# Kernel optimization log

Hardware: AMD Instinct MI355X
Metric: run time of the kernel (lower is better)

## Reference

```python
import jax, jax.numpy as jnp
import numpy as np

B, G, D, N_HEADS, FFN, L = 16, 2048, 256, 8, 1024, 4
HEAD_DIM = D // N_HEADS
EPS_LN = 1e-5
MASK_TOKEN = -10.0
REE_BASE = 100.0


def setup_inputs() -> dict:
    key = jax.random.key(0)
    ks = jax.random.split(key, 20)
    s = 0.02
    inp = {
        'x': jax.random.normal(ks[0], (B, G), jnp.float32),
        'gene_emb': jax.random.normal(ks[1], (G, D), jnp.float32) * s,
        'inv_freq': (1.0 / REE_BASE ** (jnp.arange(0, D, 2, dtype=jnp.float32) / D)),
        'Wq': jax.random.normal(ks[2], (L, D, D), jnp.float32) * s,
        'bq': jnp.zeros((L, D), jnp.float32),
        'Wk': jax.random.normal(ks[3], (L, D, D), jnp.float32) * s,
        'bk': jnp.zeros((L, D), jnp.float32),
        'Wv': jax.random.normal(ks[4], (L, D, D), jnp.float32) * s,
        'bv': jnp.zeros((L, D), jnp.float32),
        'ln1_g': jnp.ones((L, D), jnp.float32),
        'ln1_b': jnp.zeros((L, D), jnp.float32),
        'ln2_g': jnp.ones((L, D), jnp.float32),
        'ln2_b': jnp.zeros((L, D), jnp.float32),
        'WU': jax.random.normal(ks[5], (L, D, FFN), jnp.float32) * s,
        'bU': jnp.zeros((L, FFN), jnp.float32),
        'WV': jax.random.normal(ks[6], (L, FFN, D), jnp.float32) * s,
        'bV': jnp.zeros((L, D), jnp.float32),
        'Wout': jax.random.normal(ks[7], (D, 1), jnp.float32) * s,
        'bout': jnp.zeros((1,), jnp.float32),
    }
    return inp


def layernorm(x, g, b):
    m = x.mean(-1, keepdims=True)
    v = ((x - m) ** 2).mean(-1, keepdims=True)
    return (x - m) / jnp.sqrt(v + EPS_LN) * g + b


def causal_linear_attention(q, k, v):
    # q, k already feature-mapped ('sqr'); shapes [B, S, H, dh]
    b, s, h, dh = q.shape
    qs, ks_, vs = (jnp.moveaxis(t, 1, 0) for t in (q, k, v))  # [S,B,H,dh]
    num0 = jnp.zeros((b, h, dh, dh), q.dtype)
    den0 = jnp.zeros((b, h, dh), q.dtype)

    def step(carry, qkv):
        num_s, den_s = carry
        qt, kt, vt = qkv
        num_s = num_s + jnp.einsum('bhf,bhd->bhfd', kt, vt)
        den_s = den_s + kt
        num = jnp.einsum('bhf,bhfd->bhd', qt, num_s)
        den = jnp.einsum('bhf,bhf->bh', qt, den_s)
        return (num_s, den_s), num / (den[..., None] + 1e-16)

    _, out = jax.lax.scan(step, (num0, den0), (qs, ks_, vs))  # [S,B,H,dh]
    return jnp.moveaxis(out, 0, 1).reshape(b, s, h * dh)


def reference(x, gene_emb, inv_freq, Wq, bq, Wk, bk, Wv, bv,
              ln1_g, ln1_b, ln2_g, ln2_b, WU, bU, WV, bV, Wout, bout):
    b, g = x.shape
    # Rotary Expression Embedding
    freqs = x[..., None] * inv_freq  # [B,G,D/2]
    emb = jnp.concatenate([jnp.sin(freqs), jnp.cos(freqs)], axis=-1)  # [B,G,D]
    emb = jnp.where((x == MASK_TOKEN)[..., None], 0.0, emb)
    h = gene_emb[None] + emb  # [B,G,D]

    for l in range(Wq.shape[0]):
        hn = layernorm(h, ln1_g[l], ln1_b[l])  # pre-LN (on_gptln=True)
        q = (hn @ Wq[l] + bq[l]).reshape(b, g, N_HEADS, HEAD_DIM) ** 2
        k = (hn @ Wk[l] + bk[l]).reshape(b, g, N_HEADS, HEAD_DIM) ** 2
        v = (hn @ Wv[l] + bv[l]).reshape(b, g, N_HEADS, HEAD_DIM)
        h = h + causal_linear_attention(q, k, v)
        hn2 = layernorm(h, ln2_g[l], ln2_b[l])
        h = h + jax.nn.gelu(hn2 @ WU[l] + bU[l], approximate=False) @ WV[l] + bV[l]
    return (h @ Wout + bout).squeeze(-1)  # [B,G]
```

## Files before the change

kernel.cpp:

```cpp
#include <hip/hip_runtime.h>
#include <math.h>


#define GG 2048
#define DD 256
#define NROWS 32768
#define NC 32
#define CS 64

typedef __attribute__((ext_vector_type(8))) short bf16x8;
typedef __attribute__((ext_vector_type(4))) float f32x4;

struct FalseT { static constexpr bool value = false; };
struct TrueT  { static constexpr bool value = true;  };

__device__ __forceinline__ short f2bf(float f) {
  union { float f; unsigned u; } v; v.f = f;
  unsigned r = v.u + 0x7FFFu + ((v.u >> 16) & 1u);
  return (short)(r >> 16);
}
__device__ __forceinline__ float bf2f(short s) {
  union { unsigned u; float f; } v; v.u = ((unsigned)(unsigned short)s) << 16;
  return v.f;
}
__device__ __forceinline__ void gld16(const short* g, short* l) {
  __builtin_amdgcn_global_load_lds(
      (const __attribute__((address_space(1))) void*)g,
      (__attribute__((address_space(3))) void*)l, 16, 0, 0);
}
__device__ __forceinline__ float fast_gelu(float x) {
  float y = 1.595769122f * (x + 0.044715f * x * x * x);
  return x / (1.0f + __expf(-y));
}

__global__ __launch_bounds__(256) void embed_kernel(
    const float* __restrict__ x, const float* __restrict__ ge,
    const float* __restrict__ invf, float* __restrict__ h) {
  int bg = blockIdx.x * 4 + (threadIdx.x >> 6);
  int g = bg & (GG - 1);
  int lane = threadIdx.x & 63;
  float xv = x[bg];
  int d = lane * 4;
  float4 e;
  if (lane < 32) {
    float4 f = *(const float4*)&invf[d];
    e.x = sinf(xv * f.x); e.y = sinf(xv * f.y);
    e.z = sinf(xv * f.z); e.w = sinf(xv * f.w);
  } else {
    float4 f = *(const float4*)&invf[d - 128];
    e.x = cosf(xv * f.x); e.y = cosf(xv * f.y);
    e.z = cosf(xv * f.z); e.w = cosf(xv * f.w);
  }
  if (xv == -10.0f) { e.x = 0.f; e.y = 0.f; e.z = 0.f; e.w = 0.f; }
  float4 gv = *(const float4*)&ge[(size_t)g * DD + d];
  float4 o; o.x = gv.x + e.x; o.y = gv.y + e.y; o.z = gv.z + e.z; o.w = gv.w + e.w;
  *(float4*)&h[(size_t)bg * DD + d] = o;
}

__global__ __launch_bounds__(256) void ln_tiled(
    const float* __restrict__ h, const float* __restrict__ gamma,
    const float* __restrict__ beta, short* __restrict__ outT) {
  __shared__ float mean_s[32], rstd_s[32];
  __shared__ float gls[256], bls[256];
  int r0 = blockIdx.x * 32;
  int tid = threadIdx.x;
  gls[tid] = gamma[tid]; bls[tid] = beta[tid];
  {
    int row = tid >> 3, seg = tid & 7;
    const float4* hp = (const float4*)(h + (size_t)(r0 + row) * DD + seg * 32);
    float s = 0.f, s2 = 0.f;
#pragma unroll
    for (int i = 0; i < 8; ++i) {
      float4 v = hp[i];
      s += v.x + v.y + v.z + v.w;
      s2 += v.x * v.x + v.y * v.y + v.z * v.z + v.w * v.w;
    }
    s += __shfl_xor(s, 1); s += __shfl_xor(s, 2); s += __shfl_xor(s, 4);
    s2 += __shfl_xor(s2, 1); s2 += __shfl_xor(s2, 2); s2 += __shfl_xor(s2, 4);
    if (seg == 0) {
      float mn = s * (1.0f / 256.0f);
      mean_s[row] = mn;
      rstd_s[row] = rsqrtf(s2 * (1.0f / 256.0f) - mn * mn + 1e-5f);
    }
  }
  __syncthreads();
  int row = tid & 31, kc8 = (tid >> 5) & 3, half = tid >> 7;
  float mn = mean_s[row], rs = rstd_s[row];
  size_t hrow = (size_t)(r0 + row) * DD;
  int trow = (r0 & 127) + row;
  short* tb = outT + (size_t)(r0 >> 7) * 8 * 4096 + (kc8 * 128 + trow) * 8;
#pragma unroll
  for (int j = 0; j < 4; ++j) {
    int kb = half * 4 + j;
    int k0 = kb * 32 + kc8 * 8;
    float4 x0 = *(const float4*)&h[hrow + k0];
    float4 x1 = *(const float4*)&h[hrow + k0 + 4];
    float4 g0 = *(const float4*)&gls[k0], g1 = *(const float4*)&gls[k0 + 4];
    float4 b0 = *(const float4*)&bls[k0], b1 = *(const float4*)&bls[k0 + 4];
    bf16x8 aw;
    aw[0] = f2bf((x0.x - mn) * rs * g0.x + b0.x);
    aw[1] = f2bf((x0.y - mn) * rs * g0.y + b0.y);
    aw[2] = f2bf((x0.z - mn) * rs * g0.z + b0.z);
    aw[3] = f2bf((x0.w - mn) * rs * g0.w + b0.w);
    aw[4] = f2bf((x1.x - mn) * rs * g1.x + b1.x);
    aw[5] = f2bf((x1.y - mn) * rs * g1.y + b1.y);
    aw[6] = f2bf((x1.z - mn) * rs * g1.z + b1.z);
    aw[7] = f2bf((x1.w - mn) * rs * g1.w + b1.w);
    *(bf16x8*)&tb[(size_t)kb * 4096] = aw;
  }
}

__global__ __launch_bounds__(256) void prep_weights(
    const float* __restrict__ Wq, const float* __restrict__ Wk,
    const float* __restrict__ Wv, const float* __restrict__ WU,
    const float* __restrict__ WV,
    short* __restrict__ TQ, short* __restrict__ TK, short* __restrict__ TV,
    short* __restrict__ TU, short* __restrict__ TVd) {
  int zz = blockIdx.z, l = blockIdx.y;
  const float* src; short* dst; int Kd, Nd;
  if (zz == 0) { src = Wq; dst = TQ; Kd = 256; Nd = 256; }
  else if (zz == 1) { src = Wk; dst = TK; Kd = 256; Nd = 256; }
  else if (zz == 2) { src = Wv; dst = TV; Kd = 256; Nd = 256; }
  else if (zz == 3) { src = WU; dst = TU; Kd = 256; Nd = 1024; }
  else { src = WV; dst = TVd; Kd = 1024; Nd = 256; }
  int tot = Kd * Nd;
  int e = blockIdx.x * 256 + threadIdx.x;
  if (e >= tot) return;
  int t = e >> 12;
  int cslot = (e >> 3) & 511;
  int elem = e & 7;
  int kc8 = cslot >> 7, rn = cslot & 127;
  int nKb = Kd >> 5;
  int nt = t / nKb, kb = t - nt * nKb;
  int n = nt * 128 + rn, k = kb * 32 + kc8 * 8 + elem;
  dst[(size_t)l * tot + e] = f2bf(src[(size_t)l * tot + (size_t)k * Nd + n]);
}

template <int K, int EPI>
__global__ __launch_bounds__(256) void gemm_t(
    const short* __restrict__ A, const short* __restrict__ B0,
    const short* __restrict__ B1, const short* __restrict__ B2,
    const float* __restrict__ bias0, const float* __restrict__ bias1,
    const float* __restrict__ bias2,
    short* __restrict__ o0, short* __restrict__ o1, short* __restrict__ o2,
    float* __restrict__ outf, int N) {
  __shared__ __align__(16) short L[24576];
  constexpr int nIter = K / 32;
  int z = blockIdx.z;
  const short* Bt = (z == 0) ? B0 : (z == 1) ? B1 : B2;
  const float* bias = (z == 0) ? bias0 : (z == 1) ? bias1 : bias2;
  short* outz = (z == 0) ? o0 : (z == 1) ? o1 : o2;
  int m0 = blockIdx.x * 128, n0 = blockIdx.y * 128;
  int tid = threadIdx.x;
  int lane = tid & 63, w = tid >> 6;
  int q = lane >> 4, r = lane & 15;
  int wm = (w >> 1) * 64, wn = (w & 1) * 64;
  const short* At = A + (size_t)blockIdx.x * nIter * 4096;
  const short* Btl = Bt + (size_t)blockIdx.y * nIter * 4096;
  f32x4 vzero = {0.f, 0.f, 0.f, 0.f};
  f32x4 acc[4][4];
#pragma unroll
  for (int i = 0; i < 4; ++i)
#pragma unroll
    for (int j = 0; j < 4; ++j) acc[i][j] = vzero;

  int c0 = tid * 8, c1 = (tid + 256) * 8;
#pragma unroll
  for (int g = 0; g < 3; ++g) {
    gld16(At + g * 4096 + c0, &L[g * 4096 + c0]);
    gld16(At + g * 4096 + c1, &L[g * 4096 + c1]);
    gld16(Btl + g * 4096 + c0, &L[12288 + g * 4096 + c0]);
    gld16(Btl + g * 4096 + c1, &L[12288 + g * 4096 + c1]);
  }

  int abase = (q * 128 + wm + r) * 8;
  int bbase = (q * 128 + wn + r) * 8;

#pragma unroll
  for (int gi = 0; gi < nIter; ++gi) {
    const int rem = nIter - 1 - gi;
    if (rem >= 2)      __builtin_amdgcn_s_waitcnt(0x0f78);
    else if (rem == 1) __builtin_amdgcn_s_waitcnt(0x0f74);
    else               __builtin_amdgcn_s_waitcnt(0x0f70);
    __builtin_amdgcn_s_barrier();
    __builtin_amdgcn_s_setprio(1);
    const int cur = gi % 3;
    const short* Asc = &L[cur * 4096];
    const short* Bsc = &L[12288 + cur * 4096];
    bf16x8 af[4], bfr[4];
#pragma unroll
    for (int mt = 0; mt < 4; ++mt)
      af[mt] = *(const bf16x8*)&Asc[abase + mt * 16 * 8];
#pragma unroll
    for (int nt = 0; nt < 4; ++nt)
      bfr[nt] = *(const bf16x8*)&Bsc[bbase + nt * 16 * 8];
#pragma unroll
    for (int mt = 0; mt < 4; ++mt)
#pragma unroll
      for (int nt = 0; nt < 4; ++nt)
        acc[mt][nt] = __builtin_amdgcn_mfma_f32_16x16x32_bf16(bfr[nt], af[mt], acc[mt][nt], 0, 0, 0);
    __builtin_amdgcn_s_setprio(0);
    __builtin_amdgcn_s_waitcnt(0xc07f);
    __builtin_amdgcn_s_barrier();
    if (gi + 3 < nIter) {
      size_t kn = (size_t)(gi + 3) * 4096;
      gld16(At + kn + c0, &L[cur * 4096 + c0]);
      gld16(At + kn + c1, &L[cur * 4096 + c1]);
      gld16(Btl + kn + c0, &L[12288 + cur * 4096 + c0]);
      gld16(Btl + kn + c1, &L[12288 + cur * 4096 + c1]);
    }
  }

  float4 bias4[4];
#pragma unroll
  for (int nt = 0; nt < 4; ++nt) bias4[nt] = *(const float4*)&bias[n0 + wn + nt * 16 + q * 4];

  if (EPI == 0) {
    short* T = L;
#pragma unroll
    for (int mt = 0; mt < 4; ++mt) {
      int ml = wm + mt * 16 + r;
#pragma unroll
      for (int nt = 0; nt < 4; ++nt) {
        f32x4 v = acc[mt][nt];
        v[0] += bias4[nt].x; v[1] += bias4[nt].y; v[2] += bias4[nt].z; v[3] += bias4[nt].w;
        if (z < 2) { v[0] *= v[0]; v[1] *= v[1]; v[2] *= v[2]; v[3] *= v[3]; }
        short4 pk; pk.x = f2bf(v[0]); pk.y = f2bf(v[1]); pk.z = f2bf(v[2]); pk.w = f2bf(v[3]);
        *(short4*)&T[ml * 132 + wn + nt * 16 + q * 4] = pk;
      }
    }
    __syncthreads();
#pragma unroll
    for (int t2 = 0; t2 < 2; ++t2) {
      int task = tid + t2 * 256;
      int row = task & 127, hl = task >> 7;
      size_t obase = ((size_t)((n0 >> 5) + hl) * NROWS + m0 + row) * 32;
#pragma unroll
      for (int j = 0; j < 4; ++j)
        *(bf16x8*)&outz[obase + j * 8] = *(const bf16x8*)&T[row * 132 + hl * 32 + j * 8];
    }
  } else if (EPI == 1) {
#pragma unroll
    for (int mt = 0; mt < 4; ++mt) {
      int ml = wm + mt * 16 + r;
#pragma unroll
      for (int nt = 0; nt < 4; ++nt) {
        f32x4 v = acc[mt][nt];
        v[0] += bias4[nt].x; v[1] += bias4[nt].y; v[2] += bias4[nt].z; v[3] += bias4[nt].w;
#pragma unroll
        for (int e = 0; e < 4; ++e) v[e] = fast_gelu(v[e]);
        short4 o; o.x = f2bf(v[0]); o.y = f2bf(v[1]); o.z = f2bf(v[2]); o.w = f2bf(v[3]);
        int n = n0 + wn + nt * 16 + q * 4;
        size_t ti = ((size_t)blockIdx.x * (N >> 5) + (n >> 5)) * 4096 +
                    (size_t)(((n >> 3) & 3) << 10) + (ml << 3) + (n & 7);
        *(short4*)&outz[ti] = o;
      }
    }
  } else {
    float* TF = (float*)L;
#pragma unroll
    for (int half = 0; half < 2; ++half) {
      __syncthreads();
      if ((w & 1) == half) {
#pragma unroll
        for (int mt = 0; mt < 4; ++mt) {
          int ml = wm + mt * 16 + r;
#pragma unroll
          for (int nt = 0; nt < 4; ++nt) {
            f32x4 v = acc[mt][nt];
            v[0] += bias4[nt].x; v[1] += bias4[nt].y; v[2] += bias4[nt].z; v[3] += bias4[nt].w;
            *(f32x4*)&TF[ml * 68 + nt * 16 + q * 4] = v;
          }
        }
      }
      __syncthreads();
      int row = tid >> 1, col = (tid & 1) * 32;
      size_t hoff = (size_t)(m0 + row) * N + n0 + half * 64 + col;
#pragma unroll
      for (int j = 0; j < 8; ++j) {
        float4 add = *(const float4*)&TF[row * 68 + col + j * 4];
        float4 cur4 = *(float4*)&outf[hoff + j * 4];
        cur4.x += add.x; cur4.y += add.y; cur4.z += add.z; cur4.w += add.w;
        *(float4*)&outf[hoff + j * 4] = cur4;
      }
    }
  }
}

__global__ __launch_bounds__(512) void ffn_fused(
    const short* __restrict__ A, const short* __restrict__ TUw,
    const short* __restrict__ TVw, const float* __restrict__ bUp,
    const float* __restrict__ bVp, float* __restrict__ h) {
  __shared__ __align__(16) short L[81920];
  int tid = threadIdx.x;
  int lane = tid & 63, w = tid >> 6;
  int q = lane >> 4, r = lane & 15;
  int wmU = (w >> 2) * 64, wnU = (w & 3) * 32;
  int wmD = (w >> 2) * 64, wnD = (w & 3) * 64;
  const short* At = A + (size_t)blockIdx.x * 32768;

#pragma unroll
  for (int i = 0; i < 8; ++i)
    gld16(At + (i * 512 + tid) * 8, &L[(i * 512 + tid) * 8]);

  auto issueFor = [&](int t) {
    short* dst = &L[49152 + (t & 1) * 16384];
    int ss = t >> 2, pp = t & 3;
    if (pp < 2) {
      const short* g0 = TUw + ((size_t)ss * 8 + pp * 4) * 4096;
#pragma unroll
      for (int i = 0; i < 4; ++i)
        gld16(g0 + (i * 512 + tid) * 8, dst + (i * 512 + tid) * 8);
    } else {
      int kbg0 = ss * 4 + (pp - 2) * 2;
#pragma unroll
      for (int kl = 0; kl < 2; ++kl) {
        gld16(TVw + (size_t)(kbg0 + kl) * 4096 + tid * 8,
              dst + kl * 8192 + tid * 8);
        gld16(TVw + (size_t)(32 + kbg0 + kl) * 4096 + tid * 8,
              dst + kl * 8192 + 4096 + tid * 8);
      }
    }
  };

  issueFor(0); issueFor(1);

  f32x4 vzero = {0.f, 0.f, 0.f, 0.f};
  f32x4 accm[4][2], acco[4][4];
#pragma unroll
  for (int mt = 0; mt < 4; ++mt) {
#pragma unroll
    for (int nt = 0; nt < 2; ++nt) accm[mt][nt] = vzero;
#pragma unroll
    for (int nt = 0; nt < 4; ++nt) acco[mt][nt] = vzero;
  }
  float4 b4[2];

  auto slice = [&](int s, auto lastc) {
    constexpr bool LAST = decltype(lastc)::value;
#pragma unroll
    for (int p = 0; p < 2; ++p) {
      int sig = s * 4 + p;
      __builtin_amdgcn_s_waitcnt(0x0f74);
      __builtin_amdgcn_s_barrier();
      __builtin_amdgcn_s_setprio(1);
      const short* Ws = &L[49152 + (sig & 1) * 16384];
#pragma unroll
      for (int kl = 0; kl < 4; ++kl) {
        int kb = p * 4 + kl;
        bf16x8 af[4], bfr[2];
#pragma unroll
        for (int mt = 0; mt < 4; ++mt)
          af[mt] = *(const bf16x8*)&L[kb * 4096 + (q * 128 + wmU + mt * 16 + r) * 8];
#pragma unroll
        for (int nt = 0; nt < 2; ++nt)
          bfr[nt] = *(const bf16x8*)&Ws[kl * 4096 + (q * 128 + wnU + nt * 16 + r) * 8];
#pragma unroll
        for (int mt = 0; mt < 4; ++mt)
#pragma unroll
          for (int nt = 0; nt < 2; ++nt)
            accm[mt][nt] = __builtin_amdgcn_mfma_f32_16x16x32_bf16(
                bfr[nt], af[mt], accm[mt][nt], 0, 0, 0);
      }
      __builtin_amdgcn_s_setprio(0);
      if (p == 1) {
#pragma unroll
        for (int mt = 0; mt < 4; ++mt) {
          int row = wmU + mt * 16 + r;
#pragma unroll
          for (int nt = 0; nt < 2; ++nt) {
            f32x4 v = accm[mt][nt];
            float4 bb = b4[nt];
            v[0] += bb.x; v[1] += bb.y; v[2] += bb.z; v[3] += bb.w;
            short4 pk;
            pk.x = f2bf(fast_gelu(v[0])); pk.y = f2bf(fast_gelu(v[1]));
            pk.z = f2bf(fast_gelu(v[2])); pk.w = f2bf(fast_gelu(v[3]));
            int kc8 = 2 * nt + (q >> 1);
            *(short4*)&L[32768 + (w & 3) * 4096 + (kc8 * 128 + row) * 8 + (q & 1) * 4] = pk;
            accm[mt][nt] = vzero;
          }
        }
      }
      __builtin_amdgcn_s_waitcnt(0xc07f);
      __builtin_amdgcn_s_barrier();
      if (p == 0) {
        b4[0] = *(const float4*)&bUp[s * 128 + wnU + q * 4];
        b4[1] = *(const float4*)&bUp[s * 128 + wnU + 16 + q * 4];
      }
      if (sig + 2 < 32) issueFor(sig + 2);
    }
#pragma unroll
    for (int p2 = 0; p2 < 2; ++p2) {
      int sig = s * 4 + 2 + p2;
      if (LAST && p2 == 1) __builtin_amdgcn_s_waitcnt(0x0f70);
      else                 __builtin_amdgcn_s_waitcnt(0x0f74);
      __builtin_amdgcn_s_barrier();
      __builtin_amdgcn_s_setprio(1);
      const short* Ws = &L[49152 + (sig & 1) * 16384];
#pragma unroll
      for (int kl = 0; kl < 2; ++kl) {
        int mtile = p2 * 2 + kl;
        bf16x8 am[4], bvf[4];
#pragma unroll
        for (int mt = 0; mt < 4; ++mt)
          am[mt] = *(const bf16x8*)&L[32768 + mtile * 4096 + (q * 128 + wmD + mt * 16 + r) * 8];
#pragma unroll
        for (int nt = 0; nt < 4; ++nt)
          bvf[nt] = *(const bf16x8*)&Ws[kl * 8192 + (wnD >> 7) * 4096 +
                                        (q * 128 + (wnD & 127) + nt * 16 + r) * 8];
#pragma unroll
        for (int mt = 0; mt < 4; ++mt)
#pragma unroll
          for (int nt = 0; nt < 4; ++nt)
            acco[mt][nt] = __builtin_amdgcn_mfma_f32_16x16x32_bf16(
                bvf[nt], am[mt], acco[mt][nt], 0, 0, 0);
      }
      __builtin_amdgcn_s_setprio(0);
      __builtin_amdgcn_s_waitcnt(0xc07f);
      __builtin_amdgcn_s_barrier();
      if (sig + 2 < 32) issueFor(sig + 2);
    }
  };

  for (int s = 0; s < 7; ++s) slice(s, FalseT{});
  slice(7, TrueT{});

  float4 bv4[4];
#pragma unroll
  for (int nt = 0; nt < 4; ++nt) bv4[nt] = *(const float4*)&bVp[wnD + nt * 16 + q * 4];
  float* TF = (float*)L;
#pragma unroll
  for (int mt = 0; mt < 4; ++mt) {
    int row = wmD + mt * 16 + r;
#pragma unroll
    for (int nt = 0; nt < 4; ++nt) {
      f32x4 v = acco[mt][nt];
      v[0] += bv4[nt].x; v[1] += bv4[nt].y; v[2] += bv4[nt].z; v[3] += bv4[nt].w;
      *(f32x4*)&TF[row * 260 + wnD + nt * 16 + q * 4] = v;
    }
  }
  __syncthreads();
  size_t hbase = ((size_t)blockIdx.x * 128 + w * 16) * DD;
#pragma unroll
  for (int j = 0; j < 16; ++j) {
    float4 add = *(const float4*)&TF[(w * 16 + j) * 260 + lane * 4];
    float4 c4 = *(float4*)&h[hbase + (size_t)j * DD + lane * 4];
    c4.x += add.x; c4.y += add.y; c4.z += add.z; c4.w += add.w;
    *(float4*)&h[hbase + (size_t)j * DD + lane * 4] = c4;
  }
}

__global__ __launch_bounds__(256) void attn_chunk_kv(
    const short* __restrict__ Kb, const short* __restrict__ Vb,
    float* __restrict__ St, float* __restrict__ Zc) {
  __shared__ short Kt[4][32 * 72];
  __shared__ short Vt[4][32 * 72];
  int wid = threadIdx.x >> 6;
  int blk = blockIdx.x * 4 + wid;
  int c = blk & (NC - 1), bh = blk >> 5;
  int b = bh >> 3, hh = bh & 7;
  int lane = threadIdx.x & 63, q = lane >> 4, r = lane & 15;
  size_t rowbase = ((size_t)hh * NROWS + b * GG + c * CS + lane) * 32;
#pragma unroll
  for (int j = 0; j < 4; ++j) {
    bf16x8 kv = *(const bf16x8*)&Kb[rowbase + j * 8];
    bf16x8 vv = *(const bf16x8*)&Vb[rowbase + j * 8];
#pragma unroll
    for (int e = 0; e < 8; ++e) {
      Kt[wid][(j * 8 + e) * 72 + lane] = kv[e];
      Vt[wid][(j * 8 + e) * 72 + lane] = vv[e];
    }
  }
  __syncthreads();
  f32x4 vzero = {0.f, 0.f, 0.f, 0.f};
  f32x4 acc[2][2];
#pragma unroll
  for (int i = 0; i < 2; ++i)
#pragma unroll
    for (int j = 0; j < 2; ++j) acc[i][j] = vzero;
#pragma unroll
  for (int ks = 0; ks < 2; ++ks) {
    bf16x8 afr[2], bfr[2];
#pragma unroll
    for (int mt = 0; mt < 2; ++mt) afr[mt] = *(const bf16x8*)&Kt[wid][(mt * 16 + r) * 72 + ks * 32 + q * 8];
#pragma unroll
    for (int nt = 0; nt < 2; ++nt) bfr[nt] = *(const bf16x8*)&Vt[wid][(nt * 16 + r) * 72 + ks * 32 + q * 8];
#pragma unroll
    for (int mt = 0; mt < 2; ++mt)
#pragma unroll
      for (int nt = 0; nt < 2; ++nt)
        acc[mt][nt] = __builtin_amdgcn_mfma_f32_16x16x32_bf16(afr[mt], bfr[nt], acc[mt][nt], 0, 0, 0);
  }
  float* stp = St + ((size_t)bh * NC + c) * 1024;
#pragma unroll
  for (int mt = 0; mt < 2; ++mt)
#pragma unroll
    for (int nt = 0; nt < 2; ++nt)
      *(f32x4*)&stp[(nt * 16 + r) * 32 + mt * 16 + q * 4] = acc[mt][nt];
  if (lane < 32) {
    float s = 0.f;
#pragma unroll
    for (int j = 0; j < 8; ++j) {
      bf16x8 kr = *(const bf16x8*)&Kt[wid][lane * 72 + j * 8];
#pragma unroll
      for (int e = 0; e < 8; ++e) s += bf2f(kr[e]);
    }
    Zc[((size_t)bh * NC + c) * 32 + lane] = s;
  }
}

__global__ __launch_bounds__(1024) void attn_prefix(float* __restrict__ St, float* __restrict__ Zc) {
  int bh = blockIdx.x, i = threadIdx.x;
  float run = 0.f;
  float* p = St + (size_t)bh * NC * 1024 + i;
#pragma unroll
  for (int c = 0; c < NC; ++c) { float t = p[(size_t)c * 1024]; p[(size_t)c * 1024] = run; run += t; }
  if (i < 32) {
    float rz = 0.f;
    float* pz = Zc + (size_t)bh * NC * 32 + i;
#pragma unroll
    for (int c = 0; c < NC; ++c) { float t = pz[c * 32]; pz[c * 32] = rz; rz += t; }
  }
}

__global__ __launch_bounds__(256) void attn_intra(
    const short* __restrict__ Qb, const short* __restrict__ Kb,
    const short* __restrict__ Vb, const float* __restrict__ St,
    const float* __restrict__ Zc, float* __restrict__ h) {
  __shared__ __align__(16) short P[4][64 * 72];
  __shared__ short Vt[4][32 * 72];
  __shared__ float den[4][64];
  int wid = threadIdx.x >> 6;
  int u = blockIdx.x;
  int b = u >> 6, c = (u >> 1) & (NC - 1), hg = u & 1;
  int hh = hg * 4 + wid;
  int bh = b * 8 + hh;
  int lane = threadIdx.x & 63, q = lane >> 4, r = lane & 15;
  size_t hrow0 = (size_t)b * GG + c * CS;
  size_t qrow0 = (size_t)hh * NROWS + b * GG + c * CS;

  const float* zp = Zc + ((size_t)bh * NC + c) * 32;
  float qz = 0.f;
  {
    size_t qoff = (qrow0 + lane) * 32;
#pragma unroll
    for (int j = 0; j < 4; ++j) {
      bf16x8 qv = *(const bf16x8*)&Qb[qoff + j * 8];
#pragma unroll
      for (int e = 0; e < 8; ++e) qz += bf2f(qv[e]) * zp[j * 8 + e];
    }
  }
  den[wid][lane] = qz;

  {
    size_t voff = (qrow0 + lane) * 32;
#pragma unroll
    for (int j = 0; j < 4; ++j) {
      bf16x8 vv = *(const bf16x8*)&Vb[voff + j * 8];
#pragma unroll
      for (int e = 0; e < 8; ++e) Vt[wid][(j * 8 + e) * 72 + lane] = vv[e];
    }
  }

  bf16x8 ak[4], bqf[4];
#pragma unroll
  for (int t4 = 0; t4 < 4; ++t4) {
    ak[t4]  = *(const bf16x8*)&Kb[(qrow0 + t4 * 16 + r) * 32 + q * 8];
    bqf[t4] = *(const bf16x8*)&Qb[(qrow0 + t4 * 16 + r) * 32 + q * 8];
  }
  f32x4 vzero = {0.f, 0.f, 0.f, 0.f};
  f32x4 pacc[4][4];
#pragma unroll
  for (int mt = 0; mt < 4; ++mt)
#pragma unroll
    for (int nt = 0; nt < 4; ++nt)
      pacc[mt][nt] = __builtin_amdgcn_mfma_f32_16x16x32_bf16(ak[mt], bqf[nt], vzero, 0, 0, 0);

  float rs[4] = {0.f, 0.f, 0.f, 0.f};
#pragma unroll
  for (int nt = 0; nt < 4; ++nt) {
    int t = nt * 16 + r;
#pragma unroll
    for (int mt = 0; mt < 4; ++mt) {
      short4 pk;
#pragma unroll
      for (int rr = 0; rr < 4; ++rr) {
        int s = mt * 16 + q * 4 + rr;
        float pv = (s <= t) ? pacc[mt][nt][rr] : 0.f;
        rs[nt] += pv;
        ((short*)&pk)[rr] = f2bf(pv);
      }
      *(short4*)&P[wid][t * 72 + mt * 16 + q * 4] = pk;
    }
  }
#pragma unroll
  for (int nt = 0; nt < 4; ++nt) {
    rs[nt] += __shfl_xor(rs[nt], 16);
    rs[nt] += __shfl_xor(rs[nt], 32);
  }
  __syncthreads();
  if (lane < 16) {
#pragma unroll
    for (int nt = 0; nt < 4; ++nt) den[wid][nt * 16 + lane] += rs[nt];
  }
  __syncthreads();

  f32x4 oacc[4][2];
#pragma unroll
  for (int mt = 0; mt < 4; ++mt)
#pragma unroll
    for (int nt2 = 0; nt2 < 2; ++nt2) oacc[mt][nt2] = vzero;
  const float* stp = St + ((size_t)bh * NC + c) * 1024;
#pragma unroll
  for (int nt2 = 0; nt2 < 2; ++nt2) {
    float4 s0 = *(const float4*)&stp[(nt2 * 16 + r) * 32 + q * 8];
    float4 s1 = *(const float4*)&stp[(nt2 * 16 + r) * 32 + q * 8 + 4];
    bf16x8 bs;
    bs[0] = f2bf(s0.x); bs[1] = f2bf(s0.y); bs[2] = f2bf(s0.z); bs[3] = f2bf(s0.w);
    bs[4] = f2bf(s1.x); bs[5] = f2bf(s1.y); bs[6] = f2bf(s1.z); bs[7] = f2bf(s1.w);
#pragma unroll
    for (int mt = 0; mt < 4; ++mt)
      oacc[mt][nt2] = __builtin_amdgcn_mfma_f32_16x16x32_bf16(bqf[mt], bs, oacc[mt][nt2], 0, 0, 0);
  }
#pragma unroll
  for (int ks = 0; ks < 2; ++ks) {
    bf16x8 ap[4];
#pragma unroll
    for (int mt = 0; mt < 4; ++mt)
      ap[mt] = *(const bf16x8*)&P[wid][(mt * 16 + r) * 72 + ks * 32 + q * 8];
#pragma unroll
    for (int nt2 = 0; nt2 < 2; ++nt2) {
      bf16x8 bv_ = *(const bf16x8*)&Vt[wid][(nt2 * 16 + r) * 72 + ks * 32 + q * 8];
#pragma unroll
      for (int mt = 0; mt < 4; ++mt)
        oacc[mt][nt2] = __builtin_amdgcn_mfma_f32_16x16x32_bf16(ap[mt], bv_, oacc[mt][nt2], 0, 0, 0);
    }
  }

  float* OF = (float*)&P[0][0];
  __syncthreads();
#pragma unroll
  for (int mt = 0; mt < 4; ++mt) {
#pragma unroll
    for (int rr = 0; rr < 4; ++rr) {
      int t = mt * 16 + q * 4 + rr;
      float inv = 1.0f / (den[wid][t] + 1e-16f);
#pragma unroll
      for (int nt2 = 0; nt2 < 2; ++nt2)
        OF[t * 132 + wid * 32 + nt2 * 16 + r] = oacc[mt][nt2][rr] * inv;
    }
  }
  __syncthreads();
  int tid = threadIdx.x;
#pragma unroll
  for (int p = 0; p < 8; ++p) {
    int row = p * 8 + (tid >> 5);
    int f4 = (tid & 31) * 4;
    size_t off = (hrow0 + row) * DD + hg * 128 + f4;
    float4 cv = *(float4*)&h[off];
    float4 ad = *(const float4*)&OF[row * 132 + f4];
    cv.x += ad.x; cv.y += ad.y; cv.z += ad.z; cv.w += ad.w;
    *(float4*)&h[off] = cv;
  }
}

__global__ __launch_bounds__(256) void out_proj(
    const float* __restrict__ h, const float* __restrict__ Wout,
    const float* __restrict__ bout, float* __restrict__ out) {
  int row = blockIdx.x * 4 + (threadIdx.x >> 6);
  int lane = threadIdx.x & 63;
  float4 a = *(const float4*)&h[(size_t)row * DD + lane * 4];
  float4 w = *(const float4*)&Wout[lane * 4];
  float s = a.x * w.x + a.y * w.y + a.z * w.z + a.w * w.w;
#pragma unroll
  for (int o = 1; o < 64; o <<= 1) s += __shfl_xor(s, o);
  if (lane == 0) out[row] = s + bout[0];
}

extern "C" void kernel_launch(void* const* d_in, const int* in_sizes, int n_in,
                              void* d_out, int out_size, void* d_ws, size_t ws_size,
                              hipStream_t stream) {
  const float* x    = (const float*)d_in[0];
  const float* ge   = (const float*)d_in[1];
  const float* invf = (const float*)d_in[2];
  const float* Wq   = (const float*)d_in[3];
  const float* bq   = (const float*)d_in[4];
  const float* Wk   = (const float*)d_in[5];
  const float* bk   = (const float*)d_in[6];
  const float* Wv   = (const float*)d_in[7];
  const float* bv   = (const float*)d_in[8];
  const float* ln1g = (const float*)d_in[9];
  const float* ln1b = (const float*)d_in[10];
  const float* ln2g = (const float*)d_in[11];
  const float* ln2b = (const float*)d_in[12];
  const float* WU   = (const float*)d_in[13];
  const float* bU   = (const float*)d_in[14];
  const float* WV   = (const float*)d_in[15];
  const float* bV   = (const float*)d_in[16];
  const float* Wout = (const float*)d_in[17];
  const float* bout = (const float*)d_in[18];
  float* out = (float*)d_out;

  char* ws = (char*)d_ws;
  float* h   = (float*)(ws + 0);
  short* hn  = (short*)(ws + 33554432);
  char*  R   = ws + 50331648;
  short* qb  = (short*)(R + 0);
  short* kb  = (short*)(R + 16777216);
  short* vb  = (short*)(R + 33554432);
  float* St  = (float*)(R + 50331648);
  float* Zc  = (float*)(R + 67108864);
  char*  WT  = R + 67633152;
  short* TQ  = (short*)(WT + 0);
  short* TK  = (short*)(WT + 524288);
  short* TVq = (short*)(WT + 1048576);
  short* TU  = (short*)(WT + 1572864);
  short* TVd = (short*)(WT + 3670016);

  prep_weights<<<dim3(1024, 4, 5), 256, 0, stream>>>(Wq, Wk, Wv, WU, WV, TQ, TK, TVq, TU, TVd);
  embed_kernel<<<NROWS / 4, 256, 0, stream>>>(x, ge, invf, h);

  for (int l = 0; l < 4; ++l) {
    ln_tiled<<<NROWS / 32, 256, 0, stream>>>(h, ln1g + l * 256, ln1b + l * 256, hn);
    gemm_t<256, 0><<<dim3(256, 2, 3), 256, 0, stream>>>(
        hn, TQ + l * 65536, TK + l * 65536, TVq + l * 65536,
        bq + l * 256, bk + l * 256, bv + l * 256,
        qb, kb, vb, nullptr, 256);
    attn_chunk_kv<<<1024, 256, 0, stream>>>(kb, vb, St, Zc);
    attn_prefix<<<128, 1024, 0, stream>>>(St, Zc);
    attn_intra<<<1024, 256, 0, stream>>>(qb, kb, vb, St, Zc, h);
    ln_tiled<<<NROWS / 32, 256, 0, stream>>>(h, ln2g + l * 256, ln2b + l * 256, hn);
    ffn_fused<<<256, 512, 0, stream>>>(hn, TU + l * 262144, TVd + l * 262144,
                                       bU + l * 1024, bV + l * 256, h);
  }
  out_proj<<<NROWS / 4, 256, 0, stream>>>(h, Wout, bout, out);
}
```

Baseline: 753.2 us.

## Fuse layernorms into attention and FFN epilogues, widen attn_intra to all heads

Removes the separate ln_tiled launches inside the layer loop. LN2 is now computed in the attn_intra epilogue, and the next layer's LN1 in the ffn_fused epilogue, writing the bf16 tiled hn directly. For this, attn_intra processes all 8 heads per block (512 threads) so each block owns full 256-wide rows. It also drops the setprio calls in the FFN MFMA loops and changes the LDS padding stride. Each launch removed saves a full re-read of h and a kernel launch, but variance now uses E[x^2]-mean^2 and the larger attn_intra block may lower occupancy.

```diff
diff --git a/kernel.cpp b/kernel.cpp
--- a/kernel.cpp
+++ b/kernel.cpp
@@ -290,7 +290,9 @@
 __global__ __launch_bounds__(512) void ffn_fused(
     const short* __restrict__ A, const short* __restrict__ TUw,
     const short* __restrict__ TVw, const float* __restrict__ bUp,
-    const float* __restrict__ bVp, float* __restrict__ h) {
+    const float* __restrict__ bVp, float* __restrict__ h,
+    short* __restrict__ hnT, const float* __restrict__ ln1g,
+    const float* __restrict__ ln1b) {
   __shared__ __align__(16) short L[81920];
   int tid = threadIdx.x;
   int lane = tid & 63, w = tid >> 6;
@@ -343,7 +345,6 @@
       int sig = s * 4 + p;
       __builtin_amdgcn_s_waitcnt(0x0f74);
       __builtin_amdgcn_s_barrier();
-      __builtin_amdgcn_s_setprio(1);
       const short* Ws = &L[49152 + (sig & 1) * 16384];
 #pragma unroll
       for (int kl = 0; kl < 4; ++kl) {
@@ -362,7 +363,6 @@
             accm[mt][nt] = __builtin_amdgcn_mfma_f32_16x16x32_bf16(
                 bfr[nt], af[mt], accm[mt][nt], 0, 0, 0);
       }
-      __builtin_amdgcn_s_setprio(0);
       if (p == 1) {
 #pragma unroll
         for (int mt = 0; mt < 4; ++mt) {
@@ -395,7 +395,6 @@
       if (LAST && p2 == 1) __builtin_amdgcn_s_waitcnt(0x0f70);
       else                 __builtin_amdgcn_s_waitcnt(0x0f74);
       __builtin_amdgcn_s_barrier();
-      __builtin_amdgcn_s_setprio(1);
       const short* Ws = &L[49152 + (sig & 1) * 16384];
 #pragma unroll
       for (int kl = 0; kl < 2; ++kl) {
@@ -415,7 +414,6 @@
             acco[mt][nt] = __builtin_amdgcn_mfma_f32_16x16x32_bf16(
                 bvf[nt], am[mt], acco[mt][nt], 0, 0, 0);
       }
-      __builtin_amdgcn_s_setprio(0);
       __builtin_amdgcn_s_waitcnt(0xc07f);
       __builtin_amdgcn_s_barrier();
       if (sig + 2 < 32) issueFor(sig + 2);
@@ -425,10 +423,12 @@
   for (int s = 0; s < 7; ++s) slice(s, FalseT{});
   slice(7, TrueT{});
 
+  float* TF = (float*)L;
+  float* MEAN = (float*)&L[68608];
+  float* RSTD = MEAN + 128;
   float4 bv4[4];
 #pragma unroll
   for (int nt = 0; nt < 4; ++nt) bv4[nt] = *(const float4*)&bVp[wnD + nt * 16 + q * 4];
-  float* TF = (float*)L;
 #pragma unroll
   for (int mt = 0; mt < 4; ++mt) {
     int row = wmD + mt * 16 + r;
@@ -436,17 +436,57 @@
     for (int nt = 0; nt < 4; ++nt) {
       f32x4 v = acco[mt][nt];
       v[0] += bv4[nt].x; v[1] += bv4[nt].y; v[2] += bv4[nt].z; v[3] += bv4[nt].w;
-      *(f32x4*)&TF[row * 260 + wnD + nt * 16 + q * 4] = v;
+      *(f32x4*)&TF[row * 268 + wnD + nt * 16 + q * 4] = v;
     }
   }
   __syncthreads();
-  size_t hbase = ((size_t)blockIdx.x * 128 + w * 16) * DD;
-#pragma unroll
-  for (int j = 0; j < 16; ++j) {
-    float4 add = *(const float4*)&TF[(w * 16 + j) * 260 + lane * 4];
-    float4 c4 = *(float4*)&h[hbase + (size_t)j * DD + lane * 4];
-    c4.x += add.x; c4.y += add.y; c4.z += add.z; c4.w += add.w;
-    *(float4*)&h[hbase + (size_t)j * DD + lane * 4] = c4;
+#pragma unroll
+  for (int p = 0; p < 16; ++p) {
+    int row = p * 8 + w;
+    int col = lane * 4;
+    size_t off = ((size_t)blockIdx.x * 128 + row) * DD + col;
+    float4 ad = *(const float4*)&TF[row * 268 + col];
+    float4 cv = *(float4*)&h[off];
+    cv.x += ad.x; cv.y += ad.y; cv.z += ad.z; cv.w += ad.w;
+    *(float4*)&h[off] = cv;
+    if (ln1g) {
+      *(float4*)&TF[row * 268 + col] = cv;
+      float s = cv.x + cv.y + cv.z + cv.w;
+      float s2 = cv.x * cv.x + cv.y * cv.y + cv.z * cv.z + cv.w * cv.w;
+      s += __shfl_xor(s, 1); s += __shfl_xor(s, 2); s += __shfl_xor(s, 4);
+      s += __shfl_xor(s, 8); s += __shfl_xor(s, 16); s += __shfl_xor(s, 32);
+      s2 += __shfl_xor(s2, 1); s2 += __shfl_xor(s2, 2); s2 += __shfl_xor(s2, 4);
+      s2 += __shfl_xor(s2, 8); s2 += __shfl_xor(s2, 16); s2 += __shfl_xor(s2, 32);
+      if (lane == 0) {
+        float mn = s * (1.0f / 256.0f);
+        MEAN[row] = mn;
+        RSTD[row] = rsqrtf(s2 * (1.0f / 256.0f) - mn * mn + 1e-5f);
+      }
+    }
+  }
+  if (ln1g) {
+    __syncthreads();
+    int row2 = tid & 127, kc8g = tid >> 7;
+    float mn = MEAN[row2], rstd = RSTD[row2];
+    short* tb = hnT + (size_t)blockIdx.x * 32768 + (kc8g * 128 + row2) * 8;
+#pragma unroll
+    for (int kb = 0; kb < 8; ++kb) {
+      int k0 = kb * 32 + kc8g * 8;
+      float4 x0 = *(const float4*)&TF[row2 * 268 + k0];
+      float4 x1 = *(const float4*)&TF[row2 * 268 + k0 + 4];
+      float4 g0 = *(const float4*)&ln1g[k0], g1 = *(const float4*)&ln1g[k0 + 4];
+      float4 b0 = *(const float4*)&ln1b[k0], b1 = *(const float4*)&ln1b[k0 + 4];
+      bf16x8 aw;
+      aw[0] = f2bf((x0.x - mn) * rstd * g0.x + b0.x);
+      aw[1] = f2bf((x0.y - mn) * rstd * g0.y + b0.y);
+      aw[2] = f2bf((x0.z - mn) * rstd * g0.z + b0.z);
+      aw[3] = f2bf((x0.w - mn) * rstd * g0.w + b0.w);
+      aw[4] = f2bf((x1.x - mn) * rstd * g1.x + b1.x);
+      aw[5] = f2bf((x1.y - mn) * rstd * g1.y + b1.y);
+      aw[6] = f2bf((x1.z - mn) * rstd * g1.z + b1.z);
+      aw[7] = f2bf((x1.w - mn) * rstd * g1.w + b1.w);
+      *(bf16x8*)&tb[(size_t)kb * 4096] = aw;
+    }
   }
 }
 
@@ -523,18 +563,20 @@
   }
 }
 
-__global__ __launch_bounds__(256) void attn_intra(
+__global__ __launch_bounds__(512) void attn_intra(
     const short* __restrict__ Qb, const short* __restrict__ Kb,
     const short* __restrict__ Vb, const float* __restrict__ St,
-    const float* __restrict__ Zc, float* __restrict__ h) {
-  __shared__ __align__(16) short P[4][64 * 72];
-  __shared__ short Vt[4][32 * 72];
-  __shared__ float den[4][64];
+    const float* __restrict__ Zc, float* __restrict__ h,
+    short* __restrict__ hnT, const float* __restrict__ ln2g,
+    const float* __restrict__ ln2b) {
+  __shared__ __align__(16) short P[8][64 * 72];
+  __shared__ short Vt[8][32 * 72];
+  __shared__ float den[8][64];
+  __shared__ float MEAN[64], RSTD[64];
   int wid = threadIdx.x >> 6;
   int u = blockIdx.x;
-  int b = u >> 6, c = (u >> 1) & (NC - 1), hg = u & 1;
-  int hh = hg * 4 + wid;
-  int bh = b * 8 + hh;
+  int b = u >> 5, c = u & 31;
+  int hh = wid, bh = b * 8 + hh;
   int lane = threadIdx.x & 63, q = lane >> 4, r = lane & 15;
   size_t hrow0 = (size_t)b * GG + c * CS;
   size_t qrow0 = (size_t)hh * NROWS + b * GG + c * CS;
@@ -647,20 +689,56 @@
       float inv = 1.0f / (den[wid][t] + 1e-16f);
 #pragma unroll
       for (int nt2 = 0; nt2 < 2; ++nt2)
-        OF[t * 132 + wid * 32 + nt2 * 16 + r] = oacc[mt][nt2][rr] * inv;
+        OF[t * 268 + hh * 32 + nt2 * 16 + r] = oacc[mt][nt2][rr] * inv;
     }
   }
   __syncthreads();
   int tid = threadIdx.x;
 #pragma unroll
   for (int p = 0; p < 8; ++p) {
-    int row = p * 8 + (tid >> 5);
-    int f4 = (tid & 31) * 4;
-    size_t off = (hrow0 + row) * DD + hg * 128 + f4;
+    int row = p * 8 + wid;
+    int col = lane * 4;
+    size_t off = (hrow0 + row) * DD + col;
+    float4 ad = *(const float4*)&OF[row * 268 + col];
     float4 cv = *(float4*)&h[off];
-    float4 ad = *(const float4*)&OF[row * 132 + f4];
     cv.x += ad.x; cv.y += ad.y; cv.z += ad.z; cv.w += ad.w;
     *(float4*)&h[off] = cv;
+    *(float4*)&OF[row * 268 + col] = cv;
+    float s = cv.x + cv.y + cv.z + cv.w;
+    float s2 = cv.x * cv.x + cv.y * cv.y + cv.z * cv.z + cv.w * cv.w;
+    s += __shfl_xor(s, 1); s += __shfl_xor(s, 2); s += __shfl_xor(s, 4);
+    s += __shfl_xor(s, 8); s += __shfl_xor(s, 16); s += __shfl_xor(s, 32);
+    s2 += __shfl_xor(s2, 1); s2 += __shfl_xor(s2, 2); s2 += __shfl_xor(s2, 4);
+    s2 += __shfl_xor(s2, 8); s2 += __shfl_xor(s2, 16); s2 += __shfl_xor(s2, 32);
+    if (lane == 0) {
+      float mn = s * (1.0f / 256.0f);
+      MEAN[row] = mn;
+      RSTD[row] = rsqrtf(s2 * (1.0f / 256.0f) - mn * mn + 1e-5f);
+    }
+  }
+  __syncthreads();
+  int row2 = tid & 63, kc8g = (tid >> 6) & 3, half = tid >> 8;
+  float mn = MEAN[row2], rstd = RSTD[row2];
+  size_t grow = hrow0 + row2;
+  short* tb = hnT + (grow >> 7) * 32768 + (kc8g * 128 + (int)(grow & 127)) * 8;
+#pragma unroll
+  for (int j = 0; j < 4; ++j) {
+    int kb = half * 4 + j;
+    int k0 = kb * 32 + kc8g * 8;
+    float4 x0 = *(const float4*)&OF[row2 * 268 + k0];
+    float4 x1 = *(const float4*)&OF[row2 * 268 + k0 + 4];
+    float4 g0 = *(const float4*)&ln2g[k0], g1 = *(const float4*)&ln2g[k0 + 4];
+    float4 b0 = *(const float4*)&ln2b[k0], b1 = *(const float4*)&ln2b[k0 + 4];
+    bf16x8 aw;
+    aw[0] = f2bf((x0.x - mn) * rstd * g0.x + b0.x);
+    aw[1] = f2bf((x0.y - mn) * rstd * g0.y + b0.y);
+    aw[2] = f2bf((x0.z - mn) * rstd * g0.z + b0.z);
+    aw[3] = f2bf((x0.w - mn) * rstd * g0.w + b0.w);
+    aw[4] = f2bf((x1.x - mn) * rstd * g1.x + b1.x);
+    aw[5] = f2bf((x1.y - mn) * rstd * g1.y + b1.y);
+    aw[6] = f2bf((x1.z - mn) * rstd * g1.z + b1.z);
+    aw[7] = f2bf((x1.w - mn) * rstd * g1.w + b1.w);
+    *(bf16x8*)&tb[(size_t)kb * 4096] = aw;
   }
 }
 
@@ -719,19 +797,22 @@
 
   prep_weights<<<dim3(1024, 4, 5), 256, 0, stream>>>(Wq, Wk, Wv, WU, WV, TQ, TK, TVq, TU, TVd);
   embed_kernel<<<NROWS / 4, 256, 0, stream>>>(x, ge, invf, h);
+  ln_tiled<<<NROWS / 32, 256, 0, stream>>>(h, ln1g, ln1b, hn);
 
   for (int l = 0; l < 4; ++l) {
-    ln_tiled<<<NROWS / 32, 256, 0, stream>>>(h, ln1g + l * 256, ln1b + l * 256, hn);
     gemm_t<256, 0><<<dim3(256, 2, 3), 256, 0, stream>>>(
         hn, TQ + l * 65536, TK + l * 65536, TVq + l * 65536,
         bq + l * 256, bk + l * 256, bv + l * 256,
         qb, kb, vb, nullptr, 256);
     attn_chunk_kv<<<1024, 256, 0, stream>>>(kb, vb, St, Zc);
     attn_prefix<<<128, 1024, 0, stream>>>(St, Zc);
-    attn_intra<<<1024, 256, 0, stream>>>(qb, kb, vb, St, Zc, h);
-    ln_tiled<<<NROWS / 32, 256, 0, stream>>>(h, ln2g + l * 256, ln2b + l * 256, hn);
+    attn_intra<<<512, 512, 0, stream>>>(qb, kb, vb, St, Zc, h,
+                                        hn, ln2g + l * 256, ln2b + l * 256);
     ffn_fused<<<256, 512, 0, stream>>>(hn, TU + l * 262144, TVd + l * 262144,
-                                       bU + l * 1024, bV + l * 256, h);
+                                       bU + l * 1024, bV + l * 256, h,
+                                       hn,
+                                       (l < 3) ? ln1g + (l + 1) * 256 : nullptr,
+                                       (l < 3) ? ln1b + (l + 1) * 256 : nullptr);
   }
   out_proj<<<NROWS / 4, 256, 0, stream>>>(h, Wout, bout, out);
 }
```

Result: faster. 710.1 us (-5.7%).
